# Kernel optimization log

Hardware: AMD Instinct MI355X
Metric: run time of the kernel (lower is better)

Reference implementation:

```python
import jax, jax.numpy as jnp
import numpy as np

B, L, D = 2, 4096, 128      # batch, seq_len, d_model
ED = 2 * D                  # d_inner (expand=2) = 256
N = 16                      # d_state
K = 4                       # d_conv
R = (D + 15) // 16          # dt_rank = 8
H = 2 * D                   # mlp hidden = 256


def setup_inputs() -> dict:
    key = jax.random.key(0)
    ks = jax.random.split(key, 20)
    s = 0.05
    inp = {
        "x": jax.random.normal(ks[0], (B, L, D), dtype=jnp.float32),
        # outer block LayerNorm (norm1)
        "norm1_g": jnp.ones((D,), jnp.float32),
        "norm1_b": jnp.zeros((D,), jnp.float32),
        # MambaLayer inner LayerNorm
        "inner_g": jnp.ones((D,), jnp.float32),
        "inner_b": jnp.zeros((D,), jnp.float32),
        # Mamba params
        "in_w": jax.random.normal(ks[1], (2 * ED, D), jnp.float32) * s,      # in_proj (no bias)
        "conv_w": jax.random.normal(ks[2], (ED, 1, K), jnp.float32) * s,     # depthwise conv
        "conv_b": jax.random.normal(ks[3], (ED,), jnp.float32) * s,
        "xproj_w": jax.random.normal(ks[4], (R + 2 * N, ED), jnp.float32) * s,  # x_proj (no bias)
        "dt_w": jax.random.normal(ks[5], (ED, R), jnp.float32) * s,
        "dt_b": jax.random.normal(ks[6], (ED,), jnp.float32) * s,
        "A_log": jnp.tile(jnp.log(jnp.arange(1, N + 1, dtype=jnp.float32)), (ED, 1)),  # [ED,N]
        "Dp": jnp.ones((ED,), jnp.float32),
        "out_w": jax.random.normal(ks[7], (D, ED), jnp.float32) * s,         # out_proj (no bias)
        # MLP
        "fc1_w": jax.random.normal(ks[8], (H, D), jnp.float32) * s,
        "fc1_b": jnp.zeros((H,), jnp.float32),
        "fc2_w": jax.random.normal(ks[9], (D, H), jnp.float32) * s,
        "fc2_b": jnp.zeros((D,), jnp.float32),
    }
    return inp


def _ln(x, g, b, eps=1e-5):
    m = jnp.mean(x, axis=-1, keepdims=True)
    v = jnp.mean((x - m) ** 2, axis=-1, keepdims=True)
    return (x - m) * jax.lax.rsqrt(v + eps) * g + b


def _mamba(x, in_w, conv_w, conv_b, xproj_w, dt_w, dt_b, A_log, Dp, out_w):
    # x: [B, L, D]
    xz = jnp.einsum('bld,ed->ble', x, in_w)          # [B,L,2*ED]
    u, z = jnp.split(xz, 2, axis=-1)                 # each [B,L,ED]
    # causal depthwise conv1d over L
    u_c = jnp.transpose(u, (0, 2, 1))                # [B,ED,L]
    u_c = jax.lax.conv_general_dilated(
        u_c, conv_w, window_strides=(1,), padding=[(K - 1, 0)],
        dimension_numbers=('NCH', 'OIH', 'NCH'), feature_group_count=ED)
    u = jax.nn.silu(jnp.transpose(u_c, (0, 2, 1)) + conv_b)   # [B,L,ED]
    # input-dependent dt, B, C
    dbc = jnp.einsum('ble,re->blr', u, xproj_w)      # [B,L,R+2N]
    dt, Bm, Cm = jnp.split(dbc, [R, R + N], axis=-1)
    delta = jax.nn.softplus(jnp.einsum('blr,er->ble', dt, dt_w) + dt_b)  # [B,L,ED]
    A = -jnp.exp(A_log)                              # [ED,N]
    deltaA = jnp.exp(jnp.einsum('ble,en->blen', delta, A))               # [B,L,ED,N]
    deltaBu = jnp.einsum('ble,bln,ble->blen', delta, Bm, u)              # [B,L,ED,N]
    # selective scan over L
    def step(h, inp):
        dA, dBu, Ct = inp                            # [B,ED,N],[B,ED,N],[B,N]
        h = dA * h + dBu
        y = jnp.einsum('ben,bn->be', h, Ct)
        return h, y
    h0 = jnp.zeros((B, ED, N), u.dtype)
    xs = (jnp.transpose(deltaA, (1, 0, 2, 3)),
          jnp.transpose(deltaBu, (1, 0, 2, 3)),
          jnp.transpose(Cm, (1, 0, 2)))
    _, ys = jax.lax.scan(step, h0, xs)               # [L,B,ED]
    y = jnp.transpose(ys, (1, 0, 2)) + u * Dp        # [B,L,ED]
    y = y * jax.nn.silu(z)
    return jnp.einsum('ble,de->bld', y, out_w)       # [B,L,D]


def reference(x, norm1_g, norm1_b, inner_g, inner_b, in_w, conv_w, conv_b,
              xproj_w, dt_w, dt_b, A_log, Dp, out_w, fc1_w, fc1_b, fc2_w, fc2_b):
    # attn branch: mamba(inner_LN(norm1(x)))
    a = _mamba(_ln(_ln(x, norm1_g, norm1_b), inner_g, inner_b),
               in_w, conv_w, conv_b, xproj_w, dt_w, dt_b, A_log, Dp, out_w)
    x = x + a
    # mlp branch (note: original applies norm1 again to updated x)
    h = _ln(x, norm1_g, norm1_b)
    h = jax.nn.gelu(jnp.einsum('bld,hd->blh', h, fc1_w) + fc1_b, approximate=False)
    h = jnp.einsum('blh,dh->bld', h, fc2_w) + fc2_b
    return x + h
```

## Files before the change

kernel.cpp:

```cpp
#include <hip/hip_runtime.h>
#include <hip/hip_bf16.h>
#include <math.h>

#define BB 2
#define LL 4096
#define DD 128
#define ED 256
#define NN 16
#define KK 4
#define RR 8
#define HH 256
#define NT (BB*LL)
#define NC 128
#define LC 32

typedef __attribute__((ext_vector_type(8))) short short8;
typedef __attribute__((ext_vector_type(8))) unsigned short ushort8v;
typedef __attribute__((ext_vector_type(4))) float floatx4;

__device__ __forceinline__ unsigned short f2bf(float f) {
  unsigned int b = __builtin_bit_cast(unsigned int, f);
  b += 0x7FFFu + ((b >> 16) & 1u);
  return (unsigned short)(b >> 16);
}

__device__ __forceinline__ ushort8v pack8(const float4& v0, const float4& v1) {
  ushort8v p;
  p[0]=f2bf(v0.x); p[1]=f2bf(v0.y); p[2]=f2bf(v0.z); p[3]=f2bf(v0.w);
  p[4]=f2bf(v1.x); p[5]=f2bf(v1.y); p[6]=f2bf(v1.z); p[7]=f2bf(v1.w);
  return p;
}

__global__ __launch_bounds__(256) void gemm_inln_k(const float* __restrict__ x,
    const float* __restrict__ g1, const float* __restrict__ b1,
    const float* __restrict__ g2, const float* __restrict__ b2,
    const float* __restrict__ W, float* __restrict__ C) {
  __shared__ unsigned short As[64][136];
  __shared__ unsigned short Ws[64][136];
  const int row0 = blockIdx.y * 64;
  const int col0 = blockIdx.x * 64;
  const int tid  = threadIdx.x;
  const int wave = tid >> 6, lane = tid & 63;
  const int quad = lane >> 4, l16 = lane & 15;
  const int wm = (wave & 1) * 32, wn = (wave >> 1) * 32;
  const int lr = tid >> 2;
  const int lk = (tid & 3) * 32;

  {
    const float* Ap = x + (size_t)(row0 + lr)*DD + lk;
    float4 av[8];
    float s = 0.f, sq = 0.f;
    #pragma unroll
    for (int g = 0; g < 8; g++) {
      av[g] = *(const float4*)(Ap + g*4);
      s  += av[g].x + av[g].y + av[g].z + av[g].w;
      sq += av[g].x*av[g].x + av[g].y*av[g].y + av[g].z*av[g].z + av[g].w*av[g].w;
    }
    s += __shfl_xor(s, 1);  s += __shfl_xor(s, 2);
    sq += __shfl_xor(sq, 1); sq += __shfl_xor(sq, 2);
    const float m1 = s * (1.f/128.f);
    const float rs1 = rsqrtf(sq*(1.f/128.f) - m1*m1 + 1e-5f);
    float s2 = 0.f, sq2 = 0.f;
    #pragma unroll
    for (int g = 0; g < 8; g++) {
      const float4 gg = *(const float4*)(g1 + lk + g*4);
      const float4 bb = *(const float4*)(b1 + lk + g*4);
      av[g].x = (av[g].x - m1)*rs1*gg.x + bb.x;
      av[g].y = (av[g].y - m1)*rs1*gg.y + bb.y;
      av[g].z = (av[g].z - m1)*rs1*gg.z + bb.z;
      av[g].w = (av[g].w - m1)*rs1*gg.w + bb.w;
      s2  += av[g].x + av[g].y + av[g].z + av[g].w;
      sq2 += av[g].x*av[g].x + av[g].y*av[g].y + av[g].z*av[g].z + av[g].w*av[g].w;
    }
    s2 += __shfl_xor(s2, 1);  s2 += __shfl_xor(s2, 2);
    sq2 += __shfl_xor(sq2, 1); sq2 += __shfl_xor(sq2, 2);
    const float m2 = s2 * (1.f/128.f);
    const float rs2 = rsqrtf(sq2*(1.f/128.f) - m2*m2 + 1e-5f);
    #pragma unroll
    for (int g = 0; g < 4; g++) {
      const float4 ga = *(const float4*)(g2 + lk + g*8);
      const float4 gb = *(const float4*)(g2 + lk + g*8 + 4);
      const float4 ba = *(const float4*)(b2 + lk + g*8);
      const float4 bbv= *(const float4*)(b2 + lk + g*8 + 4);
      ushort8v pa;
      pa[0] = f2bf((av[2*g].x   - m2)*rs2*ga.x + ba.x);
      pa[1] = f2bf((av[2*g].y   - m2)*rs2*ga.y + ba.y);
      pa[2] = f2bf((av[2*g].z   - m2)*rs2*ga.z + ba.z);
      pa[3] = f2bf((av[2*g].w   - m2)*rs2*ga.w + ba.w);
      pa[4] = f2bf((av[2*g+1].x - m2)*rs2*gb.x + bbv.x);
      pa[5] = f2bf((av[2*g+1].y - m2)*rs2*gb.y + bbv.y);
      pa[6] = f2bf((av[2*g+1].z - m2)*rs2*gb.z + bbv.z);
      pa[7] = f2bf((av[2*g+1].w - m2)*rs2*gb.w + bbv.w);
      *(ushort8v*)&As[lr][lk + g*8] = pa;
    }
  }
  {
    const float* Wp = W + (size_t)(col0 + lr)*DD + lk;
    #pragma unroll
    for (int g = 0; g < 4; g++) {
      const float4 v0 = *(const float4*)(Wp + g*8);
      const float4 v1 = *(const float4*)(Wp + g*8 + 4);
      *(ushort8v*)&Ws[lr][lk + g*8] = pack8(v0, v1);
    }
  }
  __syncthreads();

  floatx4 acc[2][2] = {};
  #pragma unroll
  for (int ks = 0; ks < 4; ks++) {
    const int ko = ks*32 + quad*8;
    short8 a0 = *(const short8*)&As[wm +      l16][ko];
    short8 a1 = *(const short8*)&As[wm + 16 + l16][ko];
    short8 b0 = *(const short8*)&Ws[wn +      l16][ko];
    short8 b1 = *(const short8*)&Ws[wn + 16 + l16][ko];
    acc[0][0] = __builtin_amdgcn_mfma_f32_16x16x32_bf16(a0, b0, acc[0][0], 0, 0, 0);
    acc[0][1] = __builtin_amdgcn_mfma_f32_16x16x32_bf16(a0, b1, acc[0][1], 0, 0, 0);
    acc[1][0] = __builtin_amdgcn_mfma_f32_16x16x32_bf16(a1, b0, acc[1][0], 0, 0, 0);
    acc[1][1] = __builtin_amdgcn_mfma_f32_16x16x32_bf16(a1, b1, acc[1][1], 0, 0, 0);
  }
  #pragma unroll
  for (int i = 0; i < 2; i++)
    #pragma unroll
    for (int j = 0; j < 2; j++) {
      const int n = col0 + wn + j*16 + l16;
      #pragma unroll
      for (int r = 0; r < 4; r++) {
        const int m = row0 + wm + i*16 + quad*4 + r;
        C[(size_t)m*(2*ED) + n] = acc[i][j][r];
      }
    }
}

__global__ __launch_bounds__(256) void scan1f_k(
    const float* __restrict__ xz, const float* __restrict__ cw,
    const float* __restrict__ cb, const float* __restrict__ xpw,
    const float* __restrict__ dtw, const float* __restrict__ dtb,
    const float* __restrict__ A_log, float* __restrict__ uc,
    float* __restrict__ dbc, float* __restrict__ delta,
    float* __restrict__ cA, float* __restrict__ cH) {
  __shared__ __align__(16) unsigned short Bs[64][264];
  __shared__ __align__(16) unsigned short As[32][264];
  __shared__ float su[32][128];
  __shared__ float sdbc[32][40];
  float (*sdel)[128] = reinterpret_cast<float(*)[128]>(&As[0][0]);

  const int eb = blockIdx.x, c = blockIdx.y, b = blockIdx.z;
  const int tid = threadIdx.x;
  const int t0 = b*LL + c*LC;

  #pragma unroll
  for (int p = 0; p < 8; p++) {
    const int idx = p*256 + tid;
    const int row = idx >> 5;
    const int col = (idx & 31) * 8;
    ushort8v v = {};
    if (row < 40) {
      const float4 v0 = *(const float4*)(xpw + (size_t)row*ED + col);
      const float4 v1 = *(const float4*)(xpw + (size_t)row*ED + col + 4);
      v = pack8(v0, v1);
    }
    *(ushort8v*)&Bs[row][col] = v;
  }

  {
    const int ch = tid;
    const float4 w = *(const float4*)(cw + ch*4);
    const float cbe = cb[ch];
    float xv[32];
    #pragma unroll
    for (int i = 0; i < LC; i++)
      xv[i] = xz[(size_t)(t0+i)*(2*ED) + ch];
    float h0 = 0.f, h1 = 0.f, h2 = 0.f;
    if (c != 0) {
      h0 = xz[(size_t)(t0-3)*(2*ED) + ch];
      h1 = xz[(size_t)(t0-2)*(2*ED) + ch];
      h2 = xz[(size_t)(t0-1)*(2*ED) + ch];
    }
    const bool own = (ch >> 7) == eb;
    #pragma unroll
    for (int i = 0; i < LC; i++) {
      const float cur = xv[i];
      const float a = cbe + h0*w.x + h1*w.y + h2*w.z + cur*w.w;
      const float s = a / (1.f + __expf(-a));
      As[i][ch] = f2bf(s);
      if (own) {
        su[i][ch & 127] = s;
        uc[(size_t)(t0+i)*ED + ch] = s;
      }
      h0 = h1; h1 = h2; h2 = cur;
    }
  }
  __syncthreads();

  const int wave = tid >> 6, lane = tid & 63;
  const int quad = lane >> 4, l16 = lane & 15;
  {
    const int mi = (wave & 1) * 16;
    const int j0 = (wave >> 1) * 2;
    floatx4 acc[2] = {};
    #pragma unroll
    for (int ks = 0; ks < 8; ks++) {
      const int ko = ks*32 + quad*8;
      short8 a  = *(const short8*)&As[mi + l16][ko];
      short8 b0 = *(const short8*)&Bs[j0*16 +      l16][ko];
      short8 b1 = *(const short8*)&Bs[j0*16 + 16 + l16][ko];
      acc[0] = __builtin_amdgcn_mfma_f32_16x16x32_bf16(a, b0, acc[0], 0, 0, 0);
      acc[1] = __builtin_amdgcn_mfma_f32_16x16x32_bf16(a, b1, acc[1], 0, 0, 0);
    }
    __syncthreads();
    #pragma unroll
    for (int f = 0; f < 2; f++) {
      const int n = (j0 + f)*16 + l16;
      #pragma unroll
      for (int r = 0; r < 4; r++) {
        const int m = mi + quad*4 + r;
        if (n < 40) {
          sdbc[m][n] = acc[f][r];
          if (eb == 0) dbc[(size_t)(t0 + m)*40 + n] = acc[f][r];
        }
      }
    }
  }
  __syncthreads();

  const int e_loc = tid >> 1;
  const int half  = tid & 1;
  const int e     = eb*128 + e_loc;
  {
    const float4 w0 = *(const float4*)(dtw + e*RR);
    const float4 w1 = *(const float4*)(dtw + e*RR + 4);
    const float db = dtb[e];
    #pragma unroll 4
    for (int i = 0; i < 16; i++) {
      const int t = half*16 + i;
      const float a = db
          + sdbc[t][0]*w0.x + sdbc[t][1]*w0.y + sdbc[t][2]*w0.z + sdbc[t][3]*w0.w
          + sdbc[t][4]*w1.x + sdbc[t][5]*w1.y + sdbc[t][6]*w1.z + sdbc[t][7]*w1.w;
      const float d = (a > 20.f) ? a : log1pf(__expf(a));
      sdel[t][e_loc] = d;
      delta[(size_t)(t0+t)*ED + e] = d;
    }
  }
  __syncthreads();

  const int n0 = half * 8;
  const float4 a0 = *(const float4*)(A_log + e*NN + n0);
  const float4 a1 = *(const float4*)(A_log + e*NN + n0 + 4);
  float Aen[8] = {-__expf(a0.x), -__expf(a0.y), -__expf(a0.z), -__expf(a0.w),
                  -__expf(a1.x), -__expf(a1.y), -__expf(a1.z), -__expf(a1.w)};
  float h[8] = {};
  float sumd = 0.f;
  for (int i = 0; i < LC; i++) {
    const float dv = sdel[i][e_loc];
    const float du = dv * su[i][e_loc];
    const float4 B0 = *(const float4*)&sdbc[i][RR + n0];
    const float4 B1 = *(const float4*)&sdbc[i][RR + n0 + 4];
    const float Bv[8] = {B0.x,B0.y,B0.z,B0.w,B1.x,B1.y,B1.z,B1.w};
    sumd += dv;
    #pragma unroll
    for (int j = 0; j < 8; j++)
      h[j] = __expf(dv * Aen[j])*h[j] + Bv[j]*du;
  }
  const size_t base = (((size_t)c*BB + b)*ED + e)*NN + n0;
  *(float4*)(cA + base)     = make_float4(__expf(sumd*Aen[0]), __expf(sumd*Aen[1]),
                                          __expf(sumd*Aen[2]), __expf(sumd*Aen[3]));
  *(float4*)(cA + base + 4) = make_float4(__expf(sumd*Aen[4]), __expf(sumd*Aen[5]),
                                          __expf(sumd*Aen[6]), __expf(sumd*Aen[7]));
  *(float4*)(cH + base)     = make_float4(h[0], h[1], h[2], h[3]);
  *(float4*)(cH + base + 4) = make_float4(h[4], h[5], h[6], h[7]);
}

__global__ __launch_bounds__(128) void scan2_k(float* __restrict__ cA,
    const float* __restrict__ cH) {
  const int gt = blockIdx.x*128 + threadIdx.x;
  const int b = gt >> 12;
  const size_t base = (size_t)b*ED*NN + (gt & 4095);
  float h = 0.f;
  for (int g = 0; g < NC/16; g++) {
    float av[16], hv[16];
    #pragma unroll
    for (int i = 0; i < 16; i++) {
      const size_t idx = (size_t)(g*16 + i)*(BB*ED*NN) + base;
      av[i] = cA[idx]; hv[i] = cH[idx];
    }
    #pragma unroll
    for (int i = 0; i < 16; i++) {
      const size_t idx = (size_t)(g*16 + i)*(BB*ED*NN) + base;
      cA[idx] = h;
      h = av[i]*h + hv[i];
    }
  }
}

__global__ __launch_bounds__(256, 1) void tail4_k(
    const float* __restrict__ xz, const float* __restrict__ delta,
    const float* __restrict__ uc, const float* __restrict__ dbc,
    const float* __restrict__ cP, const float* __restrict__ A_log,
    const float* __restrict__ Dpv, const float* __restrict__ x,
    const float* __restrict__ g1, const float* __restrict__ b1,
    const float* __restrict__ out_w, const float* __restrict__ fc1_w,
    const float* __restrict__ fc1_b, const float* __restrict__ fc2_w,
    const float* __restrict__ fc2_b, float* __restrict__ out) {
  __shared__ __align__(16) unsigned short BigW[34816];
  __shared__ __align__(16) unsigned short Au[32][264];
  __shared__ float xs[32][132];

  const int c = blockIdx.x, b = blockIdx.y;
  const int t0 = b*LL + c*LC;
  const int tid = threadIdx.x;
  const int wave = tid >> 6, lane = tid & 63;
  const int quad = lane >> 4, l16 = lane & 15;

  {
    const int r = tid >> 1, k0 = (tid & 1) * 128;
    const float* wp = out_w + (size_t)r*ED + k0;
    #pragma unroll
    for (int g = 0; g < 16; g++) {
      const float4 v0 = *(const float4*)(wp + g*8);
      const float4 v1 = *(const float4*)(wp + g*8 + 4);
      *(ushort8v*)&BigW[(size_t)r*264 + k0 + g*8] = pack8(v0, v1);
    }
  }

  {
    const int e = tid;
    float Aen[16], h[16];
    #pragma unroll
    for (int g = 0; g < 4; g++) {
      const float4 a = *(const float4*)(A_log + e*NN + g*4);
      Aen[4*g]=-__expf(a.x); Aen[4*g+1]=-__expf(a.y);
      Aen[4*g+2]=-__expf(a.z); Aen[4*g+3]=-__expf(a.w);
      const float4 hp = *(const float4*)(cP + (((size_t)c*BB + b)*ED + e)*NN + g*4);
      h[4*g]=hp.x; h[4*g+1]=hp.y; h[4*g+2]=hp.z; h[4*g+3]=hp.w;
    }
    const float Dpe = Dpv[e];
    float pd[8], pu[8], pz[8];
    #pragma unroll
    for (int i = 0; i < 8; i++) {
      pd[i] = delta[(size_t)(t0+i)*ED + e];
      pu[i] = uc[(size_t)(t0+i)*ED + e];
      pz[i] = xz[(size_t)(t0+i)*(2*ED) + ED + e];
    }
    for (int g4 = 0; g4 < 4; g4++) {
      float cd[8], cu[8], cz[8];
      #pragma unroll
      for (int i = 0; i < 8; i++) { cd[i]=pd[i]; cu[i]=pu[i]; cz[i]=pz[i]; }
      if (g4 < 3) {
        const int tn = t0 + (g4+1)*8;
        #pragma unroll
        for (int i = 0; i < 8; i++) {
          pd[i] = delta[(size_t)(tn+i)*ED + e];
          pu[i] = uc[(size_t)(tn+i)*ED + e];
          pz[i] = xz[(size_t)(tn+i)*(2*ED) + ED + e];
        }
      }
      #pragma unroll
      for (int i = 0; i < 8; i++) {
        const int t = g4*8 + i;
        const float dv = cd[i];
        const float uv = cu[i];
        const float du = dv * uv;
        const float* bc = dbc + (size_t)(t0 + t)*40 + RR;
        const float4 B0 = *(const float4*)(bc);
        const float4 B1 = *(const float4*)(bc + 4);
        const float4 B2 = *(const float4*)(bc + 8);
        const float4 B3 = *(const float4*)(bc + 12);
        const float4 C0 = *(const float4*)(bc + 16);
        const float4 C1 = *(const float4*)(bc + 20);
        const float4 C2 = *(const float4*)(bc + 24);
        const float4 C3 = *(const float4*)(bc + 28);
        const float Bv[16] = {B0.x,B0.y,B0.z,B0.w, B1.x,B1.y,B1.z,B1.w,
                              B2.x,B2.y,B2.z,B2.w, B3.x,B3.y,B3.z,B3.w};
        const float Cv[16] = {C0.x,C0.y,C0.z,C0.w, C1.x,C1.y,C1.z,C1.w,
                              C2.x,C2.y,C2.z,C2.w, C3.x,C3.y,C3.z,C3.w};
        float part = 0.f;
        #pragma unroll
        for (int j = 0; j < 16; j++) {
          h[j] = __expf(dv * Aen[j])*h[j] + Bv[j]*du;
          part += h[j]*Cv[j];
        }
        const float g = cz[i] / (1.f + __expf(-cz[i]));
        Au[t][e] = f2bf((part + uv*Dpe) * g);
      }
    }
  }
  __syncthreads();

  {
    const int wn = wave * 32;
    floatx4 acc[2][2] = {};
    #pragma unroll
    for (int ks = 0; ks < 8; ks++) {
      const int ko = ks*32 + quad*8;
      short8 a0 = *(const short8*)&Au[l16][ko];
      short8 a1 = *(const short8*)&Au[16 + l16][ko];
      short8 b0 = *(const short8*)&BigW[(size_t)(wn +      l16)*264 + ko];
      short8 b1 = *(const short8*)&BigW[(size_t)(wn + 16 + l16)*264 + ko];
      acc[0][0] = __builtin_amdgcn_mfma_f32_16x16x32_bf16(a0, b0, acc[0][0], 0, 0, 0);
      acc[0][1] = __builtin_amdgcn_mfma_f32_16x16x32_bf16(a0, b1, acc[0][1], 0, 0, 0);
      acc[1][0] = __builtin_amdgcn_mfma_f32_16x16x32_bf16(a1, b0, acc[1][0], 0, 0, 0);
      acc[1][1] = __builtin_amdgcn_mfma_f32_16x16x32_bf16(a1, b1, acc[1][1], 0, 0, 0);
    }
    #pragma unroll
    for (int i = 0; i < 2; i++)
      #pragma unroll
      for (int j = 0; j < 2; j++) {
        const int n = wn + j*16 + l16;
        #pragma unroll
        for (int r = 0; r < 4; r++) {
          const int m = i*16 + quad*4 + r;
          xs[m][n] = acc[i][j][r] + x[(size_t)(t0 + m)*DD + n];
        }
      }
  }
  __syncthreads();

  {
    const int lr = tid >> 3, le = (tid & 7) * 16;
    float vv[16];
    float s = 0.f, sq = 0.f;
    #pragma unroll
    for (int i = 0; i < 16; i++) {
      vv[i] = xs[lr][le + i];
      s += vv[i]; sq += vv[i]*vv[i];
    }
    s += __shfl_xor(s, 1);  s += __shfl_xor(s, 2);  s += __shfl_xor(s, 4);
    sq += __shfl_xor(sq, 1); sq += __shfl_xor(sq, 2); sq += __shfl_xor(sq, 4);
    const float mean = s * (1.f/128.f);
    const float rs = rsqrtf(sq*(1.f/128.f) - mean*mean + 1e-5f);
    #pragma unroll
    for (int g = 0; g < 2; g++) {
      ushort8v p;
      #pragma unroll
      for (int i = 0; i < 8; i++) {
        const int idx = g*8 + i;
        p[i] = f2bf((vv[idx] - mean)*rs*g1[le + idx] + b1[le + idx]);
      }
      *(ushort8v*)&Au[lr][le + g*8] = p;
    }
  }
  {
    const float* wp = fc1_w + (size_t)tid*DD;
    #pragma unroll
    for (int g = 0; g < 16; g++) {
      const float4 v0 = *(const float4*)(wp + g*8);
      const float4 v1 = *(const float4*)(wp + g*8 + 4);
      *(ushort8v*)&BigW[(size_t)tid*136 + g*8] = pack8(v0, v1);
    }
  }
  __syncthreads();

  {
    const int wn = wave * 64;
    floatx4 acc[2][4] = {};
    #pragma unroll
    for (int ks = 0; ks < 4; ks++) {
      const int ko = ks*32 + quad*8;
      short8 a0 = *(const short8*)&Au[l16][ko];
      short8 a1 = *(const short8*)&Au[16 + l16][ko];
      #pragma unroll
      for (int f = 0; f < 4; f++) {
        short8 bv = *(const short8*)&BigW[(size_t)(wn + f*16 + l16)*136 + ko];
        acc[0][f] = __builtin_amdgcn_mfma_f32_16x16x32_bf16(a0, bv, acc[0][f], 0, 0, 0);
        acc[1][f] = __builtin_amdgcn_mfma_f32_16x16x32_bf16(a1, bv, acc[1][f], 0, 0, 0);
      }
    }
    __syncthreads();
    #pragma unroll
    for (int i = 0; i < 2; i++)
      #pragma unroll
      for (int f = 0; f < 4; f++) {
        const int n = wn + f*16 + l16;
        const float bn = fc1_b[n];
        #pragma unroll
        for (int r = 0; r < 4; r++) {
          const int m = i*16 + quad*4 + r;
          float v = acc[i][f][r] + bn;
          v = 0.5f*v*(1.f + erff(v*0.70710678118f));
          Au[m][n] = f2bf(v);
        }
      }
  }
  {
    const int r = tid >> 1, k0 = (tid & 1) * 128;
    const float* wp = fc2_w + (size_t)r*HH + k0;
    __syncthreads();
    #pragma unroll
    for (int g = 0; g < 16; g++) {
      const float4 v0 = *(const float4*)(wp + g*8);
      const float4 v1 = *(const float4*)(wp + g*8 + 4);
      *(ushort8v*)&BigW[(size_t)r*264 + k0 + g*8] = pack8(v0, v1);
    }
  }
  __syncthreads();

  {
    const int wn = wave * 32;
    floatx4 acc[2][2] = {};
    #pragma unroll
    for (int ks = 0; ks < 8; ks++) {
      const int ko = ks*32 + quad*8;
      short8 a0 = *(const short8*)&Au[l16][ko];
      short8 a1 = *(const short8*)&Au[16 + l16][ko];
      short8 b0 = *(const short8*)&BigW[(size_t)(wn +      l16)*264 + ko];
      short8 b1 = *(const short8*)&BigW[(size_t)(wn + 16 + l16)*264 + ko];
      acc[0][0] = __builtin_amdgcn_mfma_f32_16x16x32_bf16(a0, b0, acc[0][0], 0, 0, 0);
      acc[0][1] = __builtin_amdgcn_mfma_f32_16x16x32_bf16(a0, b1, acc[0][1], 0, 0, 0);
      acc[1][0] = __builtin_amdgcn_mfma_f32_16x16x32_bf16(a1, b0, acc[1][0], 0, 0, 0);
      acc[1][1] = __builtin_amdgcn_mfma_f32_16x16x32_bf16(a1, b1, acc[1][1], 0, 0, 0);
    }
    #pragma unroll
    for (int i = 0; i < 2; i++)
      #pragma unroll
      for (int j = 0; j < 2; j++) {
        const int n = wn + j*16 + l16;
        const float bn = fc2_b[n];
        #pragma unroll
        for (int r = 0; r < 4; r++) {
          const int m = i*16 + quad*4 + r;
          out[(size_t)(t0 + m)*DD + n] = acc[i][j][r] + bn + xs[m][n];
        }
      }
  }
}

extern "C" void kernel_launch(void* const* d_in, const int* in_sizes, int n_in,
                              void* d_out, int out_size, void* d_ws, size_t ws_size,
                              hipStream_t stream) {
  const float* x      = (const float*)d_in[0];
  const float* n1g    = (const float*)d_in[1];
  const float* n1b    = (const float*)d_in[2];
  const float* ing    = (const float*)d_in[3];
  const float* inb    = (const float*)d_in[4];
  const float* in_w   = (const float*)d_in[5];
  const float* conv_w = (const float*)d_in[6];
  const float* conv_b = (const float*)d_in[7];
  const float* xproj_w= (const float*)d_in[8];
  const float* dt_w   = (const float*)d_in[9];
  const float* dt_b   = (const float*)d_in[10];
  const float* A_log  = (const float*)d_in[11];
  const float* Dpv    = (const float*)d_in[12];
  const float* out_w  = (const float*)d_in[13];
  const float* fc1_w  = (const float*)d_in[14];
  const float* fc1_b  = (const float*)d_in[15];
  const float* fc2_w  = (const float*)d_in[16];
  const float* fc2_b  = (const float*)d_in[17];
  float* out = (float*)d_out;

  float* ws    = (float*)d_ws;
  float* xz    = ws;
  float* uc    = xz    + (size_t)NT*2*ED;
  float* dbc   = uc    + (size_t)NT*ED;
  float* delta = dbc   + (size_t)NT*40;
  float* cAP   = delta + (size_t)NT*ED;
  float* cH    = cAP   + (size_t)NC*BB*ED*NN;

  gemm_inln_k<<<dim3(512/64, NT/64), 256, 0, stream>>>(x, n1g, n1b, ing, inb, in_w, xz);
  scan1f_k<<<dim3(2, NC, BB), 256, 0, stream>>>(xz, conv_w, conv_b, xproj_w, dt_w, dt_b,
                                                A_log, uc, dbc, delta, cAP, cH);
  scan2_k<<<(BB*ED*NN)/128, 128, 0, stream>>>(cAP, cH);
  tail4_k<<<dim3(NC, BB), 256, 0, stream>>>(xz, delta, uc, dbc, cAP, A_log, Dpv,
                                            x, n1g, n1b, out_w, fc1_w, fc1_b,
                                            fc2_w, fc2_b, out);
}
```

Baseline: 187.1 us.

## Widen tail kernel to 512 threads, split scan state across thread pairs

The tail kernel moves from 256 to 512 threads. Each channel's 16-element state is split between two threads that combine partial outputs with a shuffle, and the GEMM tiles are re-partitioned across the eight waves. B/C vectors are staged in shared memory rather than reread from global per thread. The chunk scans use exp2 with log2e-prescaled A, and scan2 launches 64-thread blocks for more blocks. The trade-off is extra barriers and shuffles and smaller per-wave MFMA tiles in exchange for more parallelism in the serial scan.

```diff
diff --git a/kernel.cpp b/kernel.cpp
--- a/kernel.cpp
+++ b/kernel.cpp
@@ -14,6 +14,8 @@
 #define NC 128
 #define LC 32
 
+#define LOG2E 1.4426950408889634f
+
 typedef __attribute__((ext_vector_type(8))) short short8;
 typedef __attribute__((ext_vector_type(8))) unsigned short ushort8v;
 typedef __attribute__((ext_vector_type(4))) float floatx4;
@@ -22,6 +24,14 @@
   unsigned int b = __builtin_bit_cast(unsigned int, f);
   b += 0x7FFFu + ((b >> 16) & 1u);
   return (unsigned short)(b >> 16);
+}
+
+__device__ __forceinline__ float exp2_fast(float x) {
+#if __has_builtin(__builtin_amdgcn_exp2f)
+  return __builtin_amdgcn_exp2f(x);
+#else
+  return exp2f(x);
+#endif
 }
 
 __device__ __forceinline__ ushort8v pack8(const float4& v0, const float4& v1) {
@@ -246,8 +256,10 @@
   const int n0 = half * 8;
   const float4 a0 = *(const float4*)(A_log + e*NN + n0);
   const float4 a1 = *(const float4*)(A_log + e*NN + n0 + 4);
-  float Aen[8] = {-__expf(a0.x), -__expf(a0.y), -__expf(a0.z), -__expf(a0.w),
-                  -__expf(a1.x), -__expf(a1.y), -__expf(a1.z), -__expf(a1.w)};
+  float Aen[8] = {-__expf(a0.x)*LOG2E, -__expf(a0.y)*LOG2E,
+                  -__expf(a0.z)*LOG2E, -__expf(a0.w)*LOG2E,
+                  -__expf(a1.x)*LOG2E, -__expf(a1.y)*LOG2E,
+                  -__expf(a1.z)*LOG2E, -__expf(a1.w)*LOG2E};
   float h[8] = {};
   float sumd = 0.f;
   for (int i = 0; i < LC; i++) {
@@ -259,20 +271,20 @@
     sumd += dv;
     #pragma unroll
     for (int j = 0; j < 8; j++)
-      h[j] = __expf(dv * Aen[j])*h[j] + Bv[j]*du;
+      h[j] = exp2_fast(dv * Aen[j])*h[j] + Bv[j]*du;
   }
   const size_t base = (((size_t)c*BB + b)*ED + e)*NN + n0;
-  *(float4*)(cA + base)     = make_float4(__expf(sumd*Aen[0]), __expf(sumd*Aen[1]),
-                                          __expf(sumd*Aen[2]), __expf(sumd*Aen[3]));
-  *(float4*)(cA + base + 4) = make_float4(__expf(sumd*Aen[4]), __expf(sumd*Aen[5]),
-                                          __expf(sumd*Aen[6]), __expf(sumd*Aen[7]));
+  *(float4*)(cA + base)     = make_float4(exp2_fast(sumd*Aen[0]), exp2_fast(sumd*Aen[1]),
+                                          exp2_fast(sumd*Aen[2]), exp2_fast(sumd*Aen[3]));
+  *(float4*)(cA + base + 4) = make_float4(exp2_fast(sumd*Aen[4]), exp2_fast(sumd*Aen[5]),
+                                          exp2_fast(sumd*Aen[6]), exp2_fast(sumd*Aen[7]));
   *(float4*)(cH + base)     = make_float4(h[0], h[1], h[2], h[3]);
   *(float4*)(cH + base + 4) = make_float4(h[4], h[5], h[6], h[7]);
 }
 
-__global__ __launch_bounds__(128) void scan2_k(float* __restrict__ cA,
+__global__ __launch_bounds__(64) void scan2_k(float* __restrict__ cA,
     const float* __restrict__ cH) {
-  const int gt = blockIdx.x*128 + threadIdx.x;
+  const int gt = blockIdx.x*64 + threadIdx.x;
   const int b = gt >> 12;
   const size_t base = (size_t)b*ED*NN + (gt & 4095);
   float h = 0.f;
@@ -292,7 +304,7 @@
   }
 }
 
-__global__ __launch_bounds__(256, 1) void tail4_k(
+__global__ __launch_bounds__(512, 1) void tail5_k(
     const float* __restrict__ xz, const float* __restrict__ delta,
     const float* __restrict__ uc, const float* __restrict__ dbc,
     const float* __restrict__ cP, const float* __restrict__ A_log,
@@ -304,6 +316,7 @@
   __shared__ __align__(16) unsigned short BigW[34816];
   __shared__ __align__(16) unsigned short Au[32][264];
   __shared__ float xs[32][132];
+  __shared__ float sbc[32][32];
 
   const int c = blockIdx.x, b = blockIdx.y;
   const int t0 = b*LL + c*LC;
@@ -311,11 +324,17 @@
   const int wave = tid >> 6, lane = tid & 63;
   const int quad = lane >> 4, l16 = lane & 15;
 
-  {
-    const int r = tid >> 1, k0 = (tid & 1) * 128;
+  if (tid < 256) {
+    const int row = tid >> 3, c4 = (tid & 7) * 4;
+    *(float4*)&sbc[row][c4] = *(const float4*)(dbc + (size_t)(t0 + row)*40 + RR + c4);
+  }
+  __syncthreads();
+
+  {
+    const int r = tid >> 2, k0 = (tid & 3) * 64;
     const float* wp = out_w + (size_t)r*ED + k0;
     #pragma unroll
-    for (int g = 0; g < 16; g++) {
+    for (int g = 0; g < 8; g++) {
       const float4 v0 = *(const float4*)(wp + g*8);
       const float4 v1 = *(const float4*)(wp + g*8 + 4);
       *(ushort8v*)&BigW[(size_t)r*264 + k0 + g*8] = pack8(v0, v1);
@@ -323,15 +342,21 @@
   }
 
   {
-    const int e = tid;
-    float Aen[16], h[16];
-    #pragma unroll
-    for (int g = 0; g < 4; g++) {
-      const float4 a = *(const float4*)(A_log + e*NN + g*4);
-      Aen[4*g]=-__expf(a.x); Aen[4*g+1]=-__expf(a.y);
-      Aen[4*g+2]=-__expf(a.z); Aen[4*g+3]=-__expf(a.w);
-      const float4 hp = *(const float4*)(cP + (((size_t)c*BB + b)*ED + e)*NN + g*4);
-      h[4*g]=hp.x; h[4*g+1]=hp.y; h[4*g+2]=hp.z; h[4*g+3]=hp.w;
+    const int e = tid >> 1, half = tid & 1;
+    const int n0 = half * 8;
+    float Aen[8], h[8];
+    {
+      const float4 a0 = *(const float4*)(A_log + e*NN + n0);
+      const float4 a1 = *(const float4*)(A_log + e*NN + n0 + 4);
+      Aen[0]=-__expf(a0.x)*LOG2E; Aen[1]=-__expf(a0.y)*LOG2E;
+      Aen[2]=-__expf(a0.z)*LOG2E; Aen[3]=-__expf(a0.w)*LOG2E;
+      Aen[4]=-__expf(a1.x)*LOG2E; Aen[5]=-__expf(a1.y)*LOG2E;
+      Aen[6]=-__expf(a1.z)*LOG2E; Aen[7]=-__expf(a1.w)*LOG2E;
+      const size_t pb = (((size_t)c*BB + b)*ED + e)*NN + n0;
+      const float4 h0 = *(const float4*)(cP + pb);
+      const float4 h1 = *(const float4*)(cP + pb + 4);
+      h[0]=h0.x; h[1]=h0.y; h[2]=h0.z; h[3]=h0.w;
+      h[4]=h1.x; h[5]=h1.y; h[6]=h1.z; h[7]=h1.w;
     }
     const float Dpe = Dpv[e];
     float pd[8], pu[8], pz[8];
@@ -360,116 +385,105 @@
         const float dv = cd[i];
         const float uv = cu[i];
         const float du = dv * uv;
-        const float* bc = dbc + (size_t)(t0 + t)*40 + RR;
-        const float4 B0 = *(const float4*)(bc);
-        const float4 B1 = *(const float4*)(bc + 4);
-        const float4 B2 = *(const float4*)(bc + 8);
-        const float4 B3 = *(const float4*)(bc + 12);
-        const float4 C0 = *(const float4*)(bc + 16);
-        const float4 C1 = *(const float4*)(bc + 20);
-        const float4 C2 = *(const float4*)(bc + 24);
-        const float4 C3 = *(const float4*)(bc + 28);
-        const float Bv[16] = {B0.x,B0.y,B0.z,B0.w, B1.x,B1.y,B1.z,B1.w,
-                              B2.x,B2.y,B2.z,B2.w, B3.x,B3.y,B3.z,B3.w};
-        const float Cv[16] = {C0.x,C0.y,C0.z,C0.w, C1.x,C1.y,C1.z,C1.w,
-                              C2.x,C2.y,C2.z,C2.w, C3.x,C3.y,C3.z,C3.w};
+        const float4 B0 = *(const float4*)&sbc[t][n0];
+        const float4 B1 = *(const float4*)&sbc[t][n0 + 4];
+        const float4 C0 = *(const float4*)&sbc[t][16 + n0];
+        const float4 C1 = *(const float4*)&sbc[t][16 + n0 + 4];
+        const float Bv[8] = {B0.x,B0.y,B0.z,B0.w, B1.x,B1.y,B1.z,B1.w};
+        const float Cv[8] = {C0.x,C0.y,C0.z,C0.w, C1.x,C1.y,C1.z,C1.w};
         float part = 0.f;
         #pragma unroll
-        for (int j = 0; j < 16; j++) {
-          h[j] = __expf(dv * Aen[j])*h[j] + Bv[j]*du;
+        for (int j = 0; j < 8; j++) {
+          h[j] = exp2_fast(dv * Aen[j])*h[j] + Bv[j]*du;
           part += h[j]*Cv[j];
         }
-        const float g = cz[i] / (1.f + __expf(-cz[i]));
-        Au[t][e] = f2bf((part + uv*Dpe) * g);
-      }
-    }
-  }
-  __syncthreads();
-
-  {
-    const int wn = wave * 32;
-    floatx4 acc[2][2] = {};
+        part += __shfl_xor(part, 1);
+        if (half == 0) {
+          const float g = cz[i] / (1.f + __expf(-cz[i]));
+          Au[t][e] = f2bf((part + uv*Dpe) * g);
+        }
+      }
+    }
+  }
+  __syncthreads();
+
+  {
+    const int wn = wave * 16;
+    floatx4 acc[2] = {};
     #pragma unroll
     for (int ks = 0; ks < 8; ks++) {
       const int ko = ks*32 + quad*8;
       short8 a0 = *(const short8*)&Au[l16][ko];
       short8 a1 = *(const short8*)&Au[16 + l16][ko];
-      short8 b0 = *(const short8*)&BigW[(size_t)(wn +      l16)*264 + ko];
-      short8 b1 = *(const short8*)&BigW[(size_t)(wn + 16 + l16)*264 + ko];
+      short8 bv = *(const short8*)&BigW[(size_t)(wn + l16)*264 + ko];
+      acc[0] = __builtin_amdgcn_mfma_f32_16x16x32_bf16(a0, bv, acc[0], 0, 0, 0);
+      acc[1] = __builtin_amdgcn_mfma_f32_16x16x32_bf16(a1, bv, acc[1], 0, 0, 0);
+    }
+    #pragma unroll
+    for (int i = 0; i < 2; i++) {
+      const int n = wn + l16;
+      #pragma unroll
+      for (int r = 0; r < 4; r++) {
+        const int m = i*16 + quad*4 + r;
+        xs[m][n] = acc[i][r] + x[(size_t)(t0 + m)*DD + n];
+      }
+    }
+  }
+  __syncthreads();
+
+  {
+    const int lr = tid >> 4, le = (tid & 15) * 8;
+    float vv[8];
+    float s = 0.f, sq = 0.f;
+    #pragma unroll
+    for (int i = 0; i < 8; i++) {
+      vv[i] = xs[lr][le + i];
+      s += vv[i]; sq += vv[i]*vv[i];
+    }
+    s += __shfl_xor(s, 1);  s += __shfl_xor(s, 2);
+    s += __shfl_xor(s, 4);  s += __shfl_xor(s, 8);
+    sq += __shfl_xor(sq, 1); sq += __shfl_xor(sq, 2);
+    sq += __shfl_xor(sq, 4); sq += __shfl_xor(sq, 8);
+    const float mean = s * (1.f/128.f);
+    const float rs = rsqrtf(sq*(1.f/128.f) - mean*mean + 1e-5f);
+    ushort8v p;
+    #pragma unroll
+    for (int i = 0; i < 8; i++)
+      p[i] = f2bf((vv[i] - mean)*rs*g1[le + i] + b1[le + i]);
+    *(ushort8v*)&Au[lr][le] = p;
+  }
+  {
+    const int r = tid >> 1, k0 = (tid & 1) * 64;
+    const float* wp = fc1_w + (size_t)r*DD + k0;
+    #pragma unroll
+    for (int g = 0; g < 8; g++) {
+      const float4 v0 = *(const float4*)(wp + g*8);
+      const float4 v1 = *(const float4*)(wp + g*8 + 4);
+      *(ushort8v*)&BigW[(size_t)r*136 + k0 + g*8] = pack8(v0, v1);
+    }
+  }
+  __syncthreads();
+
+  {
+    const int wn = wave * 32;
+    floatx4 acc[2][2] = {};
+    #pragma unroll
+    for (int ks = 0; ks < 4; ks++) {
+      const int ko = ks*32 + quad*8;
+      short8 a0 = *(const short8*)&Au[l16][ko];
+      short8 a1 = *(const short8*)&Au[16 + l16][ko];
+      short8 b0 = *(const short8*)&BigW[(size_t)(wn +      l16)*136 + ko];
+      short8 b1 = *(const short8*)&BigW[(size_t)(wn + 16 + l16)*136 + ko];
       acc[0][0] = __builtin_amdgcn_mfma_f32_16x16x32_bf16(a0, b0, acc[0][0], 0, 0, 0);
       acc[0][1] = __builtin_amdgcn_mfma_f32_16x16x32_bf16(a0, b1, acc[0][1], 0, 0, 0);
       acc[1][0] = __builtin_amdgcn_mfma_f32_16x16x32_bf16(a1, b0, acc[1][0], 0, 0, 0);
       acc[1][1] = __builtin_amdgcn_mfma_f32_16x16x32_bf16(a1, b1, acc[1][1], 0, 0, 0);
     }
+    __syncthreads();
     #pragma unroll
     for (int i = 0; i < 2; i++)
       #pragma unroll
-      for (int j = 0; j < 2; j++) {
-        const int n = wn + j*16 + l16;
-        #pragma unroll
-        for (int r = 0; r < 4; r++) {
-          const int m = i*16 + quad*4 + r;
-          xs[m][n] = acc[i][j][r] + x[(size_t)(t0 + m)*DD + n];
-        }
-      }
-  }
-  __syncthreads();
-
-  {
-    const int lr = tid >> 3, le = (tid & 7) * 16;
-    float vv[16];
-    float s = 0.f, sq = 0.f;
-    #pragma unroll
-    for (int i = 0; i < 16; i++) {
-      vv[i] = xs[lr][le + i];
-      s += vv[i]; sq += vv[i]*vv[i];
-    }
-    s += __shfl_xor(s, 1);  s += __shfl_xor(s, 2);  s += __shfl_xor(s, 4);
-    sq += __shfl_xor(sq, 1); sq += __shfl_xor(sq, 2); sq += __shfl_xor(sq, 4);
-    const float mean = s * (1.f/128.f);
-    const float rs = rsqrtf(sq*(1.f/128.f) - mean*mean + 1e-5f);
-    #pragma unroll
-    for (int g = 0; g < 2; g++) {
-      ushort8v p;
-      #pragma unroll
-      for (int i = 0; i < 8; i++) {
-        const int idx = g*8 + i;
-        p[i] = f2bf((vv[idx] - mean)*rs*g1[le + idx] + b1[le + idx]);
-      }
-      *(ushort8v*)&Au[lr][le + g*8] = p;
-    }
-  }
-  {
-    const float* wp = fc1_w + (size_t)tid*DD;
-    #pragma unroll
-    for (int g = 0; g < 16; g++) {
-      const float4 v0 = *(const float4*)(wp + g*8);
-      const float4 v1 = *(const float4*)(wp + g*8 + 4);
-      *(ushort8v*)&BigW[(size_t)tid*136 + g*8] = pack8(v0, v1);
-    }
-  }
-  __syncthreads();
-
-  {
-    const int wn = wave * 64;
-    floatx4 acc[2][4] = {};
-    #pragma unroll
-    for (int ks = 0; ks < 4; ks++) {
-      const int ko = ks*32 + quad*8;
-      short8 a0 = *(const short8*)&Au[l16][ko];
-      short8 a1 = *(const short8*)&Au[16 + l16][ko];
-      #pragma unroll
-      for (int f = 0; f < 4; f++) {
-        short8 bv = *(const short8*)&BigW[(size_t)(wn + f*16 + l16)*136 + ko];
-        acc[0][f] = __builtin_amdgcn_mfma_f32_16x16x32_bf16(a0, bv, acc[0][f], 0, 0, 0);
-        acc[1][f] = __builtin_amdgcn_mfma_f32_16x16x32_bf16(a1, bv, acc[1][f], 0, 0, 0);
-      }
-    }
-    __syncthreads();
-    #pragma unroll
-    for (int i = 0; i < 2; i++)
-      #pragma unroll
-      for (int f = 0; f < 4; f++) {
+      for (int f = 0; f < 2; f++) {
         const int n = wn + f*16 + l16;
         const float bn = fc1_b[n];
         #pragma unroll
@@ -482,11 +496,11 @@
       }
   }
   {
-    const int r = tid >> 1, k0 = (tid & 1) * 128;
+    const int r = tid >> 2, k0 = (tid & 3) * 64;
     const float* wp = fc2_w + (size_t)r*HH + k0;
     __syncthreads();
     #pragma unroll
-    for (int g = 0; g < 16; g++) {
+    for (int g = 0; g < 8; g++) {
       const float4 v0 = *(const float4*)(wp + g*8);
       const float4 v1 = *(const float4*)(wp + g*8 + 4);
       *(ushort8v*)&BigW[(size_t)r*264 + k0 + g*8] = pack8(v0, v1);
@@ -495,32 +509,27 @@
   __syncthreads();
 
   {
-    const int wn = wave * 32;
-    floatx4 acc[2][2] = {};
+    const int wn = wave * 16;
+    floatx4 acc[2] = {};
     #pragma unroll
     for (int ks = 0; ks < 8; ks++) {
       const int ko = ks*32 + quad*8;
       short8 a0 = *(const short8*)&Au[l16][ko];
       short8 a1 = *(const short8*)&Au[16 + l16][ko];
-      short8 b0 = *(const short8*)&BigW[(size_t)(wn +      l16)*264 + ko];
-      short8 b1 = *(const short8*)&BigW[(size_t)(wn + 16 + l16)*264 + ko];
-      acc[0][0] = __builtin_amdgcn_mfma_f32_16x16x32_bf16(a0, b0, acc[0][0], 0, 0, 0);
-      acc[0][1] = __builtin_amdgcn_mfma_f32_16x16x32_bf16(a0, b1, acc[0][1], 0, 0, 0);
-      acc[1][0] = __builtin_amdgcn_mfma_f32_16x16x32_bf16(a1, b0, acc[1][0], 0, 0, 0);
-      acc[1][1] = __builtin_amdgcn_mfma_f32_16x16x32_bf16(a1, b1, acc[1][1], 0, 0, 0);
-    }
-    #pragma unroll
-    for (int i = 0; i < 2; i++)
-      #pragma unroll
-      for (int j = 0; j < 2; j++) {
-        const int n = wn + j*16 + l16;
-        const float bn = fc2_b[n];
-        #pragma unroll
-        for (int r = 0; r < 4; r++) {
-          const int m = i*16 + quad*4 + r;
-          out[(size_t)(t0 + m)*DD + n] = acc[i][j][r] + bn + xs[m][n];
-        }
-      }
+      short8 bv = *(const short8*)&BigW[(size_t)(wn + l16)*264 + ko];
+      acc[0] = __builtin_amdgcn_mfma_f32_16x16x32_bf16(a0, bv, acc[0], 0, 0, 0);
+      acc[1] = __builtin_amdgcn_mfma_f32_16x16x32_bf16(a1, bv, acc[1], 0, 0, 0);
+    }
+    #pragma unroll
+    for (int i = 0; i < 2; i++) {
+      const int n = wn + l16;
+      const float bn = fc2_b[n];
+      #pragma unroll
+      for (int r = 0; r < 4; r++) {
+        const int m = i*16 + quad*4 + r;
+        out[(size_t)(t0 + m)*DD + n] = acc[i][r] + bn + xs[m][n];
+      }
+    }
   }
 }
 
@@ -558,8 +567,8 @@
   gemm_inln_k<<<dim3(512/64, NT/64), 256, 0, stream>>>(x, n1g, n1b, ing, inb, in_w, xz);
   scan1f_k<<<dim3(2, NC, BB), 256, 0, stream>>>(xz, conv_w, conv_b, xproj_w, dt_w, dt_b,
                                                 A_log, uc, dbc, delta, cAP, cH);
-  scan2_k<<<(BB*ED*NN)/128, 128, 0, stream>>>(cAP, cH);
-  tail4_k<<<dim3(NC, BB), 256, 0, stream>>>(xz, delta, uc, dbc, cAP, A_log, Dpv,
+  scan2_k<<<(BB*ED*NN)/64, 64, 0, stream>>>(cAP, cH);
+  tail5_k<<<dim3(NC, BB), 512, 0, stream>>>(xz, delta, uc, dbc, cAP, A_log, Dpv,
                                             x, n1g, n1b, out_w, fc1_w, fc1_b,
                                             fc2_w, fc2_b, out);
 }
```

Result: faster. 174.6 us (-6.7%).
